# Kernel optimization log

Hardware: AMD Instinct MI355X
Metric: run time of the kernel (lower is better)

The kernel has to match this reference:

```python
import jax, jax.numpy as jnp
import numpy as np

N = 4096          # nproteins
IN_F = 512        # in_features
OUT_F = 64        # out_features
ALPHA = 0.2       # leakyrelu slope
EPS = 1e-5        # batchnorm eps
NEG = -9e15       # mask fill value from the original code


def setup_inputs() -> dict:
    key = jax.random.key(0)
    k = jax.random.split(key, 5)
    h = jax.random.normal(k[0], (N, IN_F), dtype=jnp.float32)
    # sparse 0/1 adjacency (avg degree ~20) stored dense, as the module expects
    adj = (jax.random.uniform(k[1], (N, N)) < 0.005).astype(jnp.float32)
    half = IN_F // 2
    # xavier_uniform with gain=1.414 ~ U(-b, b), b = gain*sqrt(6/(fan_in+fan_out))
    b_w = 1.414 * np.sqrt(6.0 / (half + OUT_F))
    W1 = jax.random.uniform(k[2], (half, OUT_F), minval=-b_w, maxval=b_w, dtype=jnp.float32)
    W2 = jax.random.uniform(k[3], (half, OUT_F), minval=-b_w, maxval=b_w, dtype=jnp.float32)
    b_a = 1.414 * np.sqrt(6.0 / (2 * OUT_F + 1))
    a = jax.random.uniform(k[4], (2 * OUT_F, 1), minval=-b_a, maxval=b_a, dtype=jnp.float32)
    gamma = jnp.ones((2 * OUT_F,), dtype=jnp.float32)   # bn2 weight
    beta = jnp.zeros((2 * OUT_F,), dtype=jnp.float32)   # bn2 bias
    return {"h": h, "adj": adj, "W1": W1, "W2": W2, "a": a, "gamma": gamma, "beta": beta}


def _lrelu(x):
    return jnp.where(x > 0, x, ALPHA * x)


def reference(h, adj, W1, W2, a, gamma, beta):
    d = h.shape[1] // 2
    Wh1 = h[:, :d] @ W1          # [N, F]
    Wh2 = h[:, d:] @ W2          # [N, F]

    def prep(Wh):
        s1 = Wh @ a[:OUT_F]      # [N, 1]
        s2 = Wh @ a[OUT_F:]      # [N, 1]
        return _lrelu(s1 + s2.T)  # [N, N]

    e1 = prep(Wh1)
    e2 = prep(Wh2)

    adj2 = adj @ adj                               # 2-hop counts [N, N]
    adj2 = adj2 - jnp.diag(jnp.diag(adj2))         # zero the diagonal

    att1 = jax.nn.softmax(jnp.where(adj > 0, e1, NEG), axis=1)
    h_prime1 = att1 @ Wh1                          # [N, F]
    att2 = jax.nn.softmax(jnp.where(adj2 > 0, e2, NEG), axis=1)
    h_prime2 = att2 @ Wh2                          # [N, F]

    hp = jnp.concatenate([h_prime1, h_prime2], axis=-1)  # [N, 2F]
    # BatchNorm1d (training-mode batch stats, biased variance)
    mean = hp.mean(axis=0)
    var = hp.var(axis=0)
    out = gamma * (hp - mean) / jnp.sqrt(var + EPS) + beta
    return _lrelu(out)  # concat=True branch
```

## Files before the change

kernel.cpp:

```cpp
#include <hip/hip_runtime.h>
#include <hip/hip_bf16.h>

#define NN 4096
#define IN_F 512
#define HALF 256
#define FF 64
#define ALPHA 0.2f
#define EPSV 1e-5f
#define CAP2 1024
#define H1B 1024

typedef unsigned long long u64;
typedef unsigned int u32;

__device__ __forceinline__ float lrelu(float x){ return x > 0.f ? x : ALPHA * x; }

__device__ __forceinline__ float wave_fmax(float v){
    #pragma unroll
    for (int off = 32; off; off >>= 1) v = fmaxf(v, __shfl_xor(v, off, 64));
    return v;
}
__device__ __forceinline__ float wave_fsum(float v){
    #pragma unroll
    for (int off = 32; off; off >>= 1) v += __shfl_xor(v, off, 64);
    return v;
}

__device__ __forceinline__ int build_idx(u64 bits, int lane, int cap, int* __restrict__ nbr){
    int pc = __popcll(bits);
    int scan = pc;
    #pragma unroll
    for (int off = 1; off < 64; off <<= 1) {
        int v = __shfl_up(scan, off, 64);
        if (lane >= off) scan += v;
    }
    int total = __shfl(scan, 63, 64);
    int pos = scan - pc;
    while (bits) {
        int b = __builtin_ctzll(bits);
        bits &= bits - 1;
        if (pos < cap) nbr[pos] = (lane << 6) | b;
        ++pos;
    }
    return total;
}

__global__ __launch_bounds__(256) void pack_kernel(const float* __restrict__ adj,
                                                   u64* __restrict__ packA) {
    int i = blockIdx.x;
    int tid = threadIdx.x;
    int wave = tid >> 6, lane = tid & 63;
    const float* row = adj + (size_t)i * NN;
    #pragma unroll
    for (int t = 0; t < NN / 256; ++t) {
        int col = t * 256 + tid;
        u64 m = __ballot(row[col] > 0.f);
        if (lane == 0) packA[(size_t)i * 64 + t * 4 + wave] = m;
    }
}

__global__ __launch_bounds__(128) void wh_kernel(const float* __restrict__ h,
                                                 const float* __restrict__ W1,
                                                 const float* __restrict__ W2,
                                                 const float* __restrict__ a,
                                                 float* __restrict__ Wh1,
                                                 float* __restrict__ Wh2,
                                                 float* __restrict__ s11,
                                                 float* __restrict__ s12,
                                                 float* __restrict__ s21,
                                                 float* __restrict__ s22) {
    __shared__ float hs[4 * IN_F];
    int r0 = blockIdx.x * 4;
    int tid = threadIdx.x;
    const float4* hsrc = (const float4*)(h + (size_t)r0 * IN_F);
    float4* hdst = (float4*)hs;
    #pragma unroll
    for (int t = 0; t < 4; ++t) hdst[tid + 128 * t] = hsrc[tid + 128 * t];
    __syncthreads();

    int wave = tid >> 6, f = tid & 63;
    const float* W = wave ? W2 : W1;
    const float* hw = hs + wave * HALF;
    float acc0 = 0.f, acc1 = 0.f, acc2 = 0.f, acc3 = 0.f;
    #pragma unroll 4
    for (int k = 0; k < HALF; ++k) {
        float w = W[k * FF + f];
        acc0 += hw[k] * w;
        acc1 += hw[IN_F + k] * w;
        acc2 += hw[2 * IN_F + k] * w;
        acc3 += hw[3 * IN_F + k] * w;
    }
    float* Wh = wave ? Wh2 : Wh1;
    Wh[(size_t)(r0 + 0) * FF + f] = acc0;
    Wh[(size_t)(r0 + 1) * FF + f] = acc1;
    Wh[(size_t)(r0 + 2) * FF + f] = acc2;
    Wh[(size_t)(r0 + 3) * FF + f] = acc3;

    float a1 = a[f], a2 = a[64 + f];
    #pragma unroll
    for (int r = 0; r < 4; ++r) {
        float acc = (r == 0) ? acc0 : (r == 1) ? acc1 : (r == 2) ? acc2 : acc3;
        float v1 = acc * a1, v2 = acc * a2;
        #pragma unroll
        for (int off = 32; off; off >>= 1) {
            v1 += __shfl_down(v1, off, 64);
            v2 += __shfl_down(v2, off, 64);
        }
        if (f == 0) {
            if (wave == 0) { s11[r0 + r] = v1; s12[r0 + r] = v2; }
            else           { s21[r0 + r] = v1; s22[r0 + r] = v2; }
        }
    }
}

__global__ __launch_bounds__(256) void attn_kernel(const u64* __restrict__ packA,
                                                   const float* __restrict__ Wh1,
                                                   const float* __restrict__ Wh2,
                                                   const float* __restrict__ s11,
                                                   const float* __restrict__ s12,
                                                   const float* __restrict__ s21,
                                                   const float* __restrict__ s22,
                                                   float* __restrict__ hp) {
    __shared__ int   nbr[CAP2];
    __shared__ float ev[CAP2];
    __shared__ u64   maskw[256];
    __shared__ float red[8];
    __shared__ float partial[1024];
    __shared__ int   scnt;

    int bid = blockIdx.x;
    int tid = threadIdx.x;
    int w = tid >> 6, lane = tid & 63;

    if (bid < H1B) {
        int row = bid * 4 + w;
        int*   mynbr  = nbr + w * 256;
        float* myev   = ev + w * 256;
        float* mypart = partial + w * 256;

        int total = build_idx(packA[(size_t)row * 64 + lane], lane, 256, mynbr);
        int c = min(total, 256);
        __syncthreads();

        float Z;
        if (c > 0) {
            float s11i = s11[row];
            float lm = -3.4e38f;
            for (int n = lane; n < c; n += 64) {
                float e = lrelu(s11i + s12[mynbr[n]]);
                myev[n] = e;
                lm = fmaxf(lm, e);
            }
            float m = wave_fmax(lm);
            float ls = 0.f;
            for (int n = lane; n < c; n += 64) {
                float p = __expf(myev[n] - m);
                myev[n] = p;
                ls += p;
            }
            Z = wave_fsum(ls);
        } else {
            Z = (float)NN;
        }
        __syncthreads();

        int g = lane >> 4, fq = (lane & 15) << 2;
        float ax = 0.f, ay = 0.f, az = 0.f, aw = 0.f;
        if (c > 0) {
            #pragma unroll 4
            for (int n = g; n < c; n += 4) {
                float wg = myev[n];
                const float4 v = *reinterpret_cast<const float4*>(&Wh1[(size_t)mynbr[n] * FF + fq]);
                ax += wg * v.x; ay += wg * v.y; az += wg * v.z; aw += wg * v.w;
            }
        } else {
            #pragma unroll 4
            for (int n = g; n < NN; n += 4) {
                const float4 v = *reinterpret_cast<const float4*>(&Wh1[(size_t)n * FF + fq]);
                ax += v.x; ay += v.y; az += v.z; aw += v.w;
            }
        }
        *reinterpret_cast<float4*>(&mypart[g * 64 + fq]) = make_float4(ax, ay, az, aw);
        __syncthreads();
        float s = mypart[lane] + mypart[64 + lane] + mypart[128 + lane] + mypart[192 + lane];
        hp[(size_t)row * 128 + lane] = s / Z;
    } else {
        int i = bid - H1B;
        if (w == 0) {
            int t1 = build_idx(packA[(size_t)i * 64 + lane], lane, CAP2, nbr);
            if (lane == 0) scnt = t1;
        }
        __syncthreads();
        int c1 = min(scnt, CAP2);

        u64 m = 0;
        for (int n = w; n < c1; n += 4)
            m |= packA[(size_t)nbr[n] * 64 + lane];
        maskw[w * 64 + lane] = m;
        __syncthreads();

        if (w == 0) {
            u64 word = maskw[lane] | maskw[64 + lane] | maskw[128 + lane] | maskw[192 + lane];
            if (lane == (i >> 6)) word &= ~(1ull << (i & 63));
            int t2 = build_idx(word, lane, CAP2, nbr);
            if (lane == 0) scnt = t2;
        }
        __syncthreads();
        int c2 = min(scnt, CAP2);

        float Z;
        if (c2 > 0) {
            float s21i = s21[i];
            float lm = -3.4e38f;
            for (int n = tid; n < c2; n += 256) {
                float e = lrelu(s21i + s22[nbr[n]]);
                ev[n] = e;
                lm = fmaxf(lm, e);
            }
            lm = wave_fmax(lm);
            if (lane == 0) red[w] = lm;
            __syncthreads();
            float mx = fmaxf(fmaxf(red[0], red[1]), fmaxf(red[2], red[3]));
            float ls = 0.f;
            for (int n = tid; n < c2; n += 256) {
                float p = __expf(ev[n] - mx);
                ev[n] = p;
                ls += p;
            }
            ls = wave_fsum(ls);
            if (lane == 0) red[4 + w] = ls;
            __syncthreads();
            Z = red[4] + red[5] + red[6] + red[7];
        } else {
            Z = (float)NN;
        }

        int g = tid >> 4, fq = (tid & 15) << 2;
        float ax = 0.f, ay = 0.f, az = 0.f, aw = 0.f;
        if (c2 > 0) {
            #pragma unroll 4
            for (int n = g; n < c2; n += 16) {
                float wg = ev[n];
                const float4 v = *reinterpret_cast<const float4*>(&Wh2[(size_t)nbr[n] * FF + fq]);
                ax += wg * v.x; ay += wg * v.y; az += wg * v.z; aw += wg * v.w;
            }
        } else {
            #pragma unroll 4
            for (int n = g; n < NN; n += 16) {
                const float4 v = *reinterpret_cast<const float4*>(&Wh2[(size_t)n * FF + fq]);
                ax += v.x; ay += v.y; az += v.z; aw += v.w;
            }
        }
        *reinterpret_cast<float4*>(&partial[tid << 2]) = make_float4(ax, ay, az, aw);
        __syncthreads();
        if (tid < 64) {
            float s = 0.f;
            #pragma unroll
            for (int g2 = 0; g2 < 16; ++g2) s += partial[g2 * 64 + tid];
            hp[(size_t)i * 128 + 64 + tid] = s / Z;
        }
    }
}

__global__ __launch_bounds__(256) void stats_kernel(const float* __restrict__ hp,
                                                    float* __restrict__ ps,
                                                    float* __restrict__ pq) {
    __shared__ float ls[128], lq[128];
    int tid = threadIdx.x;
    if (tid < 128) { ls[tid] = 0.f; lq[tid] = 0.f; }
    __syncthreads();
    float s0 = 0, s1 = 0, s2 = 0, s3 = 0, q0 = 0, q1 = 0, q2 = 0, q3 = 0;
    const float4* hp4 = (const float4*)hp;
    for (size_t idx = (size_t)blockIdx.x * 256 + tid; idx < (size_t)NN * 32;
         idx += (size_t)gridDim.x * 256) {
        float4 v = hp4[idx];
        s0 += v.x; q0 += v.x * v.x;
        s1 += v.y; q1 += v.y * v.y;
        s2 += v.z; q2 += v.z * v.z;
        s3 += v.w; q3 += v.w * v.w;
    }
    int cb = (tid & 31) << 2;
    atomicAdd(&ls[cb + 0], s0); atomicAdd(&lq[cb + 0], q0);
    atomicAdd(&ls[cb + 1], s1); atomicAdd(&lq[cb + 1], q1);
    atomicAdd(&ls[cb + 2], s2); atomicAdd(&lq[cb + 2], q2);
    atomicAdd(&ls[cb + 3], s3); atomicAdd(&lq[cb + 3], q3);
    __syncthreads();
    if (tid < 128) {
        ps[(size_t)blockIdx.x * 128 + tid] = ls[tid];
        pq[(size_t)blockIdx.x * 128 + tid] = lq[tid];
    }
}

__global__ __launch_bounds__(256) void finalize_kernel(const float* __restrict__ ps,
                                                       const float* __restrict__ pq,
                                                       float* __restrict__ colsum,
                                                       float* __restrict__ colsq) {
    int tid = threadIdx.x;
    const float* src = (tid < 128) ? ps : pq;
    int c = tid & 127;
    float s = 0.f;
    #pragma unroll 8
    for (int b = 0; b < 256; ++b) s += src[(size_t)b * 128 + c];
    if (tid < 128) colsum[c] = s;
    else           colsq[c]  = s;
}

__global__ __launch_bounds__(256) void norm_kernel(float* __restrict__ hp,
                                                   const float* __restrict__ colsum,
                                                   const float* __restrict__ colsq,
                                                   const float* __restrict__ gamma,
                                                   const float* __restrict__ beta) {
    size_t idx = (size_t)blockIdx.x * 256 + threadIdx.x;
    if (idx >= (size_t)NN * 32) return;
    int cb = (int)((idx << 2) & 127);
    float4 v = ((const float4*)hp)[idx];
    float r[4] = {v.x, v.y, v.z, v.w};
    #pragma unroll
    for (int t = 0; t < 4; ++t) {
        int c = cb + t;
        float mean = colsum[c] * (1.f / NN);
        float var = colsq[c] * (1.f / NN) - mean * mean;
        float inv = rsqrtf(var + EPSV);
        r[t] = lrelu((r[t] - mean) * inv * gamma[c] + beta[c]);
    }
    ((float4*)hp)[idx] = make_float4(r[0], r[1], r[2], r[3]);
}

extern "C" void kernel_launch(void* const* d_in, const int* in_sizes, int n_in,
                              void* d_out, int out_size, void* d_ws, size_t ws_size,
                              hipStream_t stream) {
    const float* h     = (const float*)d_in[0];
    const float* adj   = (const float*)d_in[1];
    const float* W1    = (const float*)d_in[2];
    const float* W2    = (const float*)d_in[3];
    const float* a     = (const float*)d_in[4];
    const float* gamma = (const float*)d_in[5];
    const float* beta  = (const float*)d_in[6];
    float* hp = (float*)d_out;

    u64* packA  = (u64*)d_ws;
    float* Wh1  = (float*)(packA + (size_t)NN * 64);
    float* Wh2  = Wh1 + (size_t)NN * FF;
    float* s11  = Wh2 + (size_t)NN * FF;
    float* s12  = s11 + NN;
    float* s21  = s12 + NN;
    float* s22  = s21 + NN;
    float* ps   = s22 + NN;
    float* pq   = ps + 256 * 128;
    float* colsum = pq + 256 * 128;
    float* colsq  = colsum + 128;

    pack_kernel<<<NN, 256, 0, stream>>>(adj, packA);
    wh_kernel<<<NN / 4, 128, 0, stream>>>(h, W1, W2, a, Wh1, Wh2, s11, s12, s21, s22);
    attn_kernel<<<H1B + NN, 256, 0, stream>>>(packA, Wh1, Wh2, s11, s12, s21, s22, hp);
    stats_kernel<<<256, 256, 0, stream>>>(hp, ps, pq);
    finalize_kernel<<<1, 256, 0, stream>>>(ps, pq, colsum, colsq);
    norm_kernel<<<(NN * 32 + 255) / 256, 256, 0, stream>>>(hp, colsum, colsq, gamma, beta);
}
```

Baseline: 191.2 us.

## Fuse hop-1 and hop-2 attention into one block per row

```diff
diff --git a/kernel.cpp b/kernel.cpp
--- a/kernel.cpp
+++ b/kernel.cpp
@@ -7,8 +7,8 @@
 #define FF 64
 #define ALPHA 0.2f
 #define EPSV 1e-5f
+#define CAP1 256
 #define CAP2 1024
-#define H1B 1024
 
 typedef unsigned long long u64;
 typedef unsigned int u32;
@@ -121,144 +121,133 @@
                                                    const float* __restrict__ s21,
                                                    const float* __restrict__ s22,
                                                    float* __restrict__ hp) {
-    __shared__ int   nbr[CAP2];
-    __shared__ float ev[CAP2];
-    __shared__ u64   maskw[256];
+    __shared__ int   nbr1[CAP1];
+    __shared__ float ev1[CAP1];
+    __shared__ int   nbr2[CAP2];
+    __shared__ float ev2[CAP2];
+    __shared__ u64   maskw[3 * 64];
     __shared__ float red[8];
     __shared__ float partial[1024];
-    __shared__ int   scnt;
-
-    int bid = blockIdx.x;
+    __shared__ int   scnt1, scnt2;
+
+    int i = blockIdx.x;
     int tid = threadIdx.x;
     int w = tid >> 6, lane = tid & 63;
 
-    if (bid < H1B) {
-        int row = bid * 4 + w;
-        int*   mynbr  = nbr + w * 256;
-        float* myev   = ev + w * 256;
-        float* mypart = partial + w * 256;
-
-        int total = build_idx(packA[(size_t)row * 64 + lane], lane, 256, mynbr);
-        int c = min(total, 256);
-        __syncthreads();
-
-        float Z;
-        if (c > 0) {
-            float s11i = s11[row];
+    if (w == 0) {
+        int t1 = build_idx(packA[(size_t)i * 64 + lane], lane, CAP1, nbr1);
+        if (lane == 0) scnt1 = t1;
+    }
+    __syncthreads();
+    int c1 = min(scnt1, CAP1);
+
+    if (c1 > 0) {
+        if (w == 0) {
+            float s11i = s11[i];
             float lm = -3.4e38f;
-            for (int n = lane; n < c; n += 64) {
-                float e = lrelu(s11i + s12[mynbr[n]]);
-                myev[n] = e;
+            for (int n = lane; n < c1; n += 64) {
+                float e = lrelu(s11i + s12[nbr1[n]]);
+                ev1[n] = e;
                 lm = fmaxf(lm, e);
             }
             float m = wave_fmax(lm);
             float ls = 0.f;
-            for (int n = lane; n < c; n += 64) {
-                float p = __expf(myev[n] - m);
-                myev[n] = p;
+            for (int n = lane; n < c1; n += 64) {
+                float p = __expf(ev1[n] - m);
+                ev1[n] = p;
                 ls += p;
             }
-            Z = wave_fsum(ls);
+            float Z = wave_fsum(ls);
+            float acc = 0.f;
+            #pragma unroll 4
+            for (int n = 0; n < c1; ++n)
+                acc += ev1[n] * Wh1[(size_t)nbr1[n] * FF + lane];
+            hp[(size_t)i * 128 + lane] = acc / Z;
         } else {
-            Z = (float)NN;
-        }
-        __syncthreads();
-
-        int g = lane >> 4, fq = (lane & 15) << 2;
-        float ax = 0.f, ay = 0.f, az = 0.f, aw = 0.f;
-        if (c > 0) {
-            #pragma unroll 4
-            for (int n = g; n < c; n += 4) {
-                float wg = myev[n];
-                const float4 v = *reinterpret_cast<const float4*>(&Wh1[(size_t)mynbr[n] * FF + fq]);
-                ax += wg * v.x; ay += wg * v.y; az += wg * v.z; aw += wg * v.w;
-            }
-        } else {
-            #pragma unroll 4
-            for (int n = g; n < NN; n += 4) {
-                const float4 v = *reinterpret_cast<const float4*>(&Wh1[(size_t)n * FF + fq]);
-                ax += v.x; ay += v.y; az += v.z; aw += v.w;
-            }
-        }
-        *reinterpret_cast<float4*>(&mypart[g * 64 + fq]) = make_float4(ax, ay, az, aw);
-        __syncthreads();
-        float s = mypart[lane] + mypart[64 + lane] + mypart[128 + lane] + mypart[192 + lane];
-        hp[(size_t)row * 128 + lane] = s / Z;
+            u64 m = 0;
+            for (int n = w - 1; n < c1; n += 3)
+                m |= packA[(size_t)nbr1[n] * 64 + lane];
+            maskw[(w - 1) * 64 + lane] = m;
+        }
     } else {
-        int i = bid - H1B;
-        if (w == 0) {
-            int t1 = build_idx(packA[(size_t)i * 64 + lane], lane, CAP2, nbr);
-            if (lane == 0) scnt = t1;
-        }
-        __syncthreads();
-        int c1 = min(scnt, CAP2);
-
-        u64 m = 0;
-        for (int n = w; n < c1; n += 4)
-            m |= packA[(size_t)nbr[n] * 64 + lane];
-        maskw[w * 64 + lane] = m;
-        __syncthreads();
-
-        if (w == 0) {
-            u64 word = maskw[lane] | maskw[64 + lane] | maskw[128 + lane] | maskw[192 + lane];
-            if (lane == (i >> 6)) word &= ~(1ull << (i & 63));
-            int t2 = build_idx(word, lane, CAP2, nbr);
-            if (lane == 0) scnt = t2;
-        }
-        __syncthreads();
-        int c2 = min(scnt, CAP2);
-
-        float Z;
-        if (c2 > 0) {
-            float s21i = s21[i];
-            float lm = -3.4e38f;
-            for (int n = tid; n < c2; n += 256) {
-                float e = lrelu(s21i + s22[nbr[n]]);
-                ev[n] = e;
-                lm = fmaxf(lm, e);
-            }
-            lm = wave_fmax(lm);
-            if (lane == 0) red[w] = lm;
-            __syncthreads();
-            float mx = fmaxf(fmaxf(red[0], red[1]), fmaxf(red[2], red[3]));
-            float ls = 0.f;
-            for (int n = tid; n < c2; n += 256) {
-                float p = __expf(ev[n] - mx);
-                ev[n] = p;
-                ls += p;
-            }
-            ls = wave_fsum(ls);
-            if (lane == 0) red[4 + w] = ls;
-            __syncthreads();
-            Z = red[4] + red[5] + red[6] + red[7];
-        } else {
-            Z = (float)NN;
-        }
-
         int g = tid >> 4, fq = (tid & 15) << 2;
         float ax = 0.f, ay = 0.f, az = 0.f, aw = 0.f;
-        if (c2 > 0) {
-            #pragma unroll 4
-            for (int n = g; n < c2; n += 16) {
-                float wg = ev[n];
-                const float4 v = *reinterpret_cast<const float4*>(&Wh2[(size_t)nbr[n] * FF + fq]);
-                ax += wg * v.x; ay += wg * v.y; az += wg * v.z; aw += wg * v.w;
-            }
-        } else {
-            #pragma unroll 4
-            for (int n = g; n < NN; n += 16) {
-                const float4 v = *reinterpret_cast<const float4*>(&Wh2[(size_t)n * FF + fq]);
-                ax += v.x; ay += v.y; az += v.z; aw += v.w;
-            }
+        for (int n = g; n < NN; n += 16) {
+            const float4 v = *reinterpret_cast<const float4*>(&Wh1[(size_t)n * FF + fq]);
+            ax += v.x; ay += v.y; az += v.z; aw += v.w;
         }
         *reinterpret_cast<float4*>(&partial[tid << 2]) = make_float4(ax, ay, az, aw);
+        if (w) maskw[(w - 1) * 64 + lane] = 0;
         __syncthreads();
         if (tid < 64) {
             float s = 0.f;
             #pragma unroll
             for (int g2 = 0; g2 < 16; ++g2) s += partial[g2 * 64 + tid];
-            hp[(size_t)i * 128 + 64 + tid] = s / Z;
-        }
+            hp[(size_t)i * 128 + tid] = s / (float)NN;
+        }
+    }
+    __syncthreads();
+
+    if (w == 0) {
+        u64 word = maskw[lane] | maskw[64 + lane] | maskw[128 + lane];
+        if (lane == (i >> 6)) word &= ~(1ull << (i & 63));
+        int t2 = build_idx(word, lane, CAP2, nbr2);
+        if (lane == 0) scnt2 = t2;
+    }
+    __syncthreads();
+    int c2 = min(scnt2, CAP2);
+
+    float Z2;
+    if (c2 > 0) {
+        float s21i = s21[i];
+        float lm = -3.4e38f;
+        for (int n = tid; n < c2; n += 256) {
+            float e = lrelu(s21i + s22[nbr2[n]]);
+            ev2[n] = e;
+            lm = fmaxf(lm, e);
+        }
+        lm = wave_fmax(lm);
+        if (lane == 0) red[w] = lm;
+        __syncthreads();
+        float mx = fmaxf(fmaxf(red[0], red[1]), fmaxf(red[2], red[3]));
+        float ls = 0.f;
+        for (int n = tid; n < c2; n += 256) {
+            float p = __expf(ev2[n] - mx);
+            ev2[n] = p;
+            ls += p;
+        }
+        ls = wave_fsum(ls);
+        if (lane == 0) red[4 + w] = ls;
+        __syncthreads();
+        Z2 = red[4] + red[5] + red[6] + red[7];
+    } else {
+        Z2 = (float)NN;
+    }
+
+    int g = tid >> 4, fq = (tid & 15) << 2;
+    float ax = 0.f, ay = 0.f, az = 0.f, aw = 0.f;
+    if (c2 > 0) {
+        #pragma unroll 4
+        for (int n = g; n < c2; n += 16) {
+            float wg = ev2[n];
+            const float4 v = *reinterpret_cast<const float4*>(&Wh2[(size_t)nbr2[n] * FF + fq]);
+            ax += wg * v.x; ay += wg * v.y; az += wg * v.z; aw += wg * v.w;
+        }
+    } else {
+        #pragma unroll 4
+        for (int n = g; n < NN; n += 16) {
+            const float4 v = *reinterpret_cast<const float4*>(&Wh2[(size_t)n * FF + fq]);
+            ax += v.x; ay += v.y; az += v.z; aw += v.w;
+        }
+    }
+    __syncthreads();
+    *reinterpret_cast<float4*>(&partial[tid << 2]) = make_float4(ax, ay, az, aw);
+    __syncthreads();
+    if (tid < 64) {
+        float s = 0.f;
+        #pragma unroll
+        for (int g2 = 0; g2 < 16; ++g2) s += partial[g2 * 64 + tid];
+        hp[(size_t)i * 128 + 64 + tid] = s / Z2;
     }
 }
 
@@ -352,7 +341,7 @@
 
     pack_kernel<<<NN, 256, 0, stream>>>(adj, packA);
     wh_kernel<<<NN / 4, 128, 0, stream>>>(h, W1, W2, a, Wh1, Wh2, s11, s12, s21, s22);
-    attn_kernel<<<H1B + NN, 256, 0, stream>>>(packA, Wh1, Wh2, s11, s12, s21, s22, hp);
+    attn_kernel<<<NN, 256, 0, stream>>>(packA, Wh1, Wh2, s11, s12, s21, s22, hp);
     stats_kernel<<<256, 256, 0, stream>>>(hp, ps, pq);
     finalize_kernel<<<1, 256, 0, stream>>>(ps, pq, colsum, colsq);
     norm_kernel<<<(NN * 32 + 255) / 256, 256, 0, stream>>>(hp, colsum, colsq, gamma, beta);
```

Result: faster. 179.2 us (-6.3%).
